# Kernel tuning notes

Hardware: AMD Instinct MI355X
Metric: run time of the kernel (lower is better)

The kernel has to match this reference:

```python
import jax, jax.numpy as jnp
import numpy as np

G = 512      # number of structures (groups)
CNT = 8192   # residues per structure
S = 8192     # sampled pairs per structure (self.samples)
N = G * CNT  # total residues


def _sample_pairs():
    # Deterministic replication of StochasticRGNLoss.pairs: per-group randint
    # sampling, with group offsets added so indices address the global array.
    rng = np.random.default_rng(0)
    local = rng.integers(0, CNT, size=(G, S, 2))
    # avoid degenerate left==right pairs (zero distance -> NaN grad of norm)
    eq = local[..., 0] == local[..., 1]
    local[..., 1] = np.where(eq, (local[..., 1] + 1) % CNT, local[..., 1])
    offs = (np.arange(G) * CNT)[:, None, None]
    pairs = (local + offs).reshape(-1, 2)
    return pairs[:, 0].astype(np.int32), pairs[:, 1].astype(np.int32)


def setup_inputs() -> dict:
    key = jax.random.key(0)
    k1, k2 = jax.random.split(key)
    inputs = jax.random.normal(k1, (N, 3, 3), dtype=jnp.float32)
    target = jax.random.normal(k2, (N, 3, 3), dtype=jnp.float32)
    left_np, right_np = _sample_pairs()
    return {
        "inputs": inputs,
        "target": target,
        "left": jnp.asarray(left_np),
        "right": jnp.asarray(right_np),
    }


def reference(inputs, target, left, right):
    # take the CA atom (index 1) of each residue frame -> [N, 3]
    ca_in = inputs[:, 1]
    ca_tg = target[:, 1]
    # irregular gather of sampled pairs, pairwise distances -> [P]
    d_in = jnp.linalg.norm(ca_in[left] - ca_in[right], axis=1)
    d_tg = jnp.linalg.norm(ca_tg[left] - ca_tg[right], axis=1)
    return jnp.mean((d_in - d_tg) ** 2)
```

## Files before the change

kernel.cpp:

```cpp
#include <hip/hip_runtime.h>

#define G_GROUPS 512
#define CNT      8192
#define S_PAIRS  8192
#define BLOCK    1024

union F4H {
    float4   f;
    _Float16 h[8];
};

__global__ __launch_bounds__(BLOCK) void rgn_loss_kernel(
    const float* __restrict__ inputs,
    const float* __restrict__ target,
    const int*   __restrict__ left,
    const int*   __restrict__ right,
    float*       __restrict__ out)
{
    __shared__ float4 pts[CNT];
    __shared__ float  red[BLOCK / 64];

    const int g   = blockIdx.x;
    const int tid = threadIdx.x;
    const int gbase = g * CNT;

    for (int p = tid; p < CNT; p += BLOCK) {
        const size_t rec = (size_t)(gbase + p) * 9 + 3;
        const float* pin = inputs + rec;
        const float* ptg = target + rec;
        F4H u;
        u.h[0] = (_Float16)pin[0];
        u.h[1] = (_Float16)pin[1];
        u.h[2] = (_Float16)pin[2];
        u.h[3] = (_Float16)ptg[0];
        u.h[4] = (_Float16)ptg[1];
        u.h[5] = (_Float16)ptg[2];
        u.h[6] = (_Float16)0.0f;
        u.h[7] = (_Float16)0.0f;
        pts[p] = u.f;
    }
    __syncthreads();

    const size_t pbase = (size_t)g * S_PAIRS;
    float acc = 0.0f;
    for (int k = tid; k < S_PAIRS; k += BLOCK) {
        const int li = left [pbase + k] - gbase;
        const int ri = right[pbase + k] - gbase;
        F4H L, R;
        L.f = pts[li];
        R.f = pts[ri];
        const float dix = (float)L.h[0] - (float)R.h[0];
        const float diy = (float)L.h[1] - (float)R.h[1];
        const float diz = (float)L.h[2] - (float)R.h[2];
        const float dtx = (float)L.h[3] - (float)R.h[3];
        const float dty = (float)L.h[4] - (float)R.h[4];
        const float dtz = (float)L.h[5] - (float)R.h[5];
        const float din = sqrtf(dix * dix + diy * diy + diz * diz);
        const float dtg = sqrtf(dtx * dtx + dty * dty + dtz * dtz);
        const float d   = din - dtg;
        acc += d * d;
    }

    const int lane = tid & 63;
    const int wid  = tid >> 6;
    #pragma unroll
    for (int off = 32; off > 0; off >>= 1)
        acc += __shfl_down(acc, off);
    if (lane == 0) red[wid] = acc;
    __syncthreads();
    if (wid == 0) {
        float v = (lane < BLOCK / 64) ? red[lane] : 0.0f;
        #pragma unroll
        for (int off = 8; off > 0; off >>= 1)
            v += __shfl_down(v, off);
        if (lane == 0)
            atomicAdd(out, v * (1.0f / ((float)G_GROUPS * (float)S_PAIRS)));
    }
}

extern "C" void kernel_launch(void* const* d_in, const int* in_sizes, int n_in,
                              void* d_out, int out_size, void* d_ws, size_t ws_size,
                              hipStream_t stream) {
    const float* inputs = (const float*)d_in[0];
    const float* target = (const float*)d_in[1];
    const int*   left   = (const int*)d_in[2];
    const int*   right  = (const int*)d_in[3];
    float*       out    = (float*)d_out;

    hipMemsetAsync(out, 0, sizeof(float), stream);
    rgn_loss_kernel<<<G_GROUPS, BLOCK, 0, stream>>>(inputs, target, left, right, out);
}
```

Before: 334.4 us.

## Stage residue records via coalesced float4 loads through per-wave LDS bounce buffer

Each wave now loads whole 9-float residue records as contiguous float4 chunks, stages them in a per-wave shared-memory bounce buffer, and extracts the CA coordinates from there. The old path issued strided scalar loads. The point table is packed to 6 halves (12 bytes) per residue instead of 16, which shrinks LDS. Pair indices are prefetched into registers before staging so their latency overlaps the gather. In exchange the kernel reads the full 36-byte records, including unused atoms, and the bounce buffer uses more LDS. The packed layout also needs three 4-byte LDS reads per point instead of one 16-byte read.

```diff
diff --git a/kernel.cpp b/kernel.cpp
--- a/kernel.cpp
+++ b/kernel.cpp
@@ -4,72 +4,99 @@
 #define CNT      8192
 #define S_PAIRS  8192
 #define BLOCK    1024
+#define WAVES    (BLOCK / 64)
+#define REC_PER_WAVE (CNT / WAVES)
+#define SUB_REC  64
+#define SUB_ITERS (REC_PER_WAVE / SUB_REC)
+#define SUB_F4   (SUB_REC * 9 / 4)
+#define PAIRS_PER_THREAD (S_PAIRS / BLOCK)
 
-union F4H {
-    float4   f;
-    _Float16 h[8];
+union U2H {
+    unsigned int u;
+    _Float16     h[2];
 };
 
 __global__ __launch_bounds__(BLOCK) void rgn_loss_kernel(
-    const float* __restrict__ inputs,
-    const float* __restrict__ target,
-    const int*   __restrict__ left,
-    const int*   __restrict__ right,
-    float*       __restrict__ out)
+    const float4* __restrict__ inputs4,
+    const float4* __restrict__ target4,
+    const int*    __restrict__ left,
+    const int*    __restrict__ right,
+    float*        __restrict__ out)
 {
-    __shared__ float4 pts[CNT];
-    __shared__ float  red[BLOCK / 64];
+    __shared__ _Float16 ptsH[CNT * 6];
+    __shared__ float4 bounce4[WAVES * SUB_F4];
+    __shared__ float red[WAVES];
 
-    const int g   = blockIdx.x;
-    const int tid = threadIdx.x;
+    const int tid  = threadIdx.x;
+    const int lane = tid & 63;
+    const int wid  = tid >> 6;
+    const int g    = blockIdx.x;
     const int gbase = g * CNT;
 
-    for (int p = tid; p < CNT; p += BLOCK) {
-        const size_t rec = (size_t)(gbase + p) * 9 + 3;
-        const float* pin = inputs + rec;
-        const float* ptg = target + rec;
-        F4H u;
-        u.h[0] = (_Float16)pin[0];
-        u.h[1] = (_Float16)pin[1];
-        u.h[2] = (_Float16)pin[2];
-        u.h[3] = (_Float16)ptg[0];
-        u.h[4] = (_Float16)ptg[1];
-        u.h[5] = (_Float16)ptg[2];
-        u.h[6] = (_Float16)0.0f;
-        u.h[7] = (_Float16)0.0f;
-        pts[p] = u.f;
+    const size_t pbase = (size_t)g * S_PAIRS;
+    int li[PAIRS_PER_THREAD], ri[PAIRS_PER_THREAD];
+    #pragma unroll
+    for (int i = 0; i < PAIRS_PER_THREAD; ++i) {
+        li[i] = left [pbase + tid + i * BLOCK] - gbase;
+        ri[i] = right[pbase + tid + i * BLOCK] - gbase;
+    }
+
+    float4* myb4 = &bounce4[wid * SUB_F4];
+    const float* myb = (const float*)myb4;
+
+    #pragma unroll
+    for (int t = 0; t < 2; ++t) {
+        const float4* src = (t == 0) ? inputs4 : target4;
+        const size_t wbase_f4 = ((size_t)gbase + (size_t)wid * REC_PER_WAVE) * 9 / 4;
+        for (int s = 0; s < SUB_ITERS; ++s) {
+            const size_t cbase = wbase_f4 + (size_t)s * SUB_F4;
+            float4 v0 = src[cbase + lane];
+            float4 v1 = src[cbase + lane + 64];
+            float4 v2;
+            if (lane < SUB_F4 - 128) v2 = src[cbase + lane + 128];
+            myb4[lane]      = v0;
+            myb4[lane + 64] = v1;
+            if (lane < SUB_F4 - 128) myb4[lane + 128] = v2;
+            const float x = myb[9 * lane + 3];
+            const float y = myb[9 * lane + 4];
+            const float z = myb[9 * lane + 5];
+            const int p = wid * REC_PER_WAVE + s * SUB_REC + lane;
+            _Float16* dst = &ptsH[p * 6 + t * 3];
+            dst[0] = (_Float16)x;
+            dst[1] = (_Float16)y;
+            dst[2] = (_Float16)z;
+        }
     }
     __syncthreads();
 
-    const size_t pbase = (size_t)g * S_PAIRS;
+    const unsigned int* ptsU = (const unsigned int*)ptsH;
     float acc = 0.0f;
-    for (int k = tid; k < S_PAIRS; k += BLOCK) {
-        const int li = left [pbase + k] - gbase;
-        const int ri = right[pbase + k] - gbase;
-        F4H L, R;
-        L.f = pts[li];
-        R.f = pts[ri];
-        const float dix = (float)L.h[0] - (float)R.h[0];
-        const float diy = (float)L.h[1] - (float)R.h[1];
-        const float diz = (float)L.h[2] - (float)R.h[2];
-        const float dtx = (float)L.h[3] - (float)R.h[3];
-        const float dty = (float)L.h[4] - (float)R.h[4];
-        const float dtz = (float)L.h[5] - (float)R.h[5];
+    #pragma unroll
+    for (int i = 0; i < PAIRS_PER_THREAD; ++i) {
+        const int l3 = li[i] * 3;
+        const int r3 = ri[i] * 3;
+        U2H L0, L1, L2, R0, R1, R2;
+        L0.u = ptsU[l3];     L1.u = ptsU[l3 + 1]; L2.u = ptsU[l3 + 2];
+        R0.u = ptsU[r3];     R1.u = ptsU[r3 + 1]; R2.u = ptsU[r3 + 2];
+        const float dix = (float)L0.h[0] - (float)R0.h[0];
+        const float diy = (float)L0.h[1] - (float)R0.h[1];
+        const float diz = (float)L1.h[0] - (float)R1.h[0];
+        const float dtx = (float)L1.h[1] - (float)R1.h[1];
+        const float dty = (float)L2.h[0] - (float)R2.h[0];
+        const float dtz = (float)L2.h[1] - (float)R2.h[1];
         const float din = sqrtf(dix * dix + diy * diy + diz * diz);
         const float dtg = sqrtf(dtx * dtx + dty * dty + dtz * dtz);
         const float d   = din - dtg;
         acc += d * d;
     }
 
-    const int lane = tid & 63;
-    const int wid  = tid >> 6;
     #pragma unroll
     for (int off = 32; off > 0; off >>= 1)
         acc += __shfl_down(acc, off);
     if (lane == 0) red[wid] = acc;
     __syncthreads();
     if (wid == 0) {
-        float v = (lane < BLOCK / 64) ? red[lane] : 0.0f;
+        float v = (lane < WAVES) ? red[lane] : 0.0f;
         #pragma unroll
         for (int off = 8; off > 0; off >>= 1)
             v += __shfl_down(v, off);
@@ -81,11 +108,11 @@
 extern "C" void kernel_launch(void* const* d_in, const int* in_sizes, int n_in,
                               void* d_out, int out_size, void* d_ws, size_t ws_size,
                               hipStream_t stream) {
-    const float* inputs = (const float*)d_in[0];
-    const float* target = (const float*)d_in[1];
-    const int*   left   = (const int*)d_in[2];
-    const int*   right  = (const int*)d_in[3];
-    float*       out    = (float*)d_out;
+    const float4* inputs = (const float4*)d_in[0];
+    const float4* target = (const float4*)d_in[1];
+    const int*    left   = (const int*)d_in[2];
+    const int*    right  = (const int*)d_in[3];
+    float*        out    = (float*)d_out;
 
     hipMemsetAsync(out, 0, sizeof(float), stream);
     rgn_loss_kernel<<<G_GROUPS, BLOCK, 0, stream>>>(inputs, target, left, right, out);
```

Result: no change. 338.9 us (+1.3%).

## Stage CA coordinates into LDS via direct global-to-LDS loads in two phases

Applied to the files above, without the earlier changes.

Replaces the per-thread scalar loads plus fp16 packing with __builtin_amdgcn_global_load_lds 16-byte copies of the CA record (reading 4 floats, one spilling past the CA triple) straight into shared memory, first for inputs, then reusing the same table for target. Pair indices are prefetched into registers before staging so their latency overlaps the table fill. This removes the fp16 conversion, keeping full fp32 precision, and halves the scalar load instructions, at the cost of extra barriers and serialising the two table phases. The 16-byte reads are unaligned (offset 12 bytes times 9-float stride), which the direct-to-LDS path may or may not support correctly.

```diff
diff --git a/kernel.cpp b/kernel.cpp
--- a/kernel.cpp
+++ b/kernel.cpp
@@ -4,11 +4,13 @@
 #define CNT      8192
 #define S_PAIRS  8192
 #define BLOCK    1024
+#define WAVES    (BLOCK / 64)
+#define RPW      (CNT / WAVES)
+#define CHUNKS   (RPW / 64)
+#define PPT      (S_PAIRS / BLOCK)
 
-union F4H {
-    float4   f;
-    _Float16 h[8];
-};
+typedef __attribute__((address_space(3))) void  lds_void;
+typedef const __attribute__((address_space(1))) void g_void;
 
 __global__ __launch_bounds__(BLOCK) void rgn_loss_kernel(
     const float* __restrict__ inputs,
@@ -17,59 +19,80 @@
     const int*   __restrict__ right,
     float*       __restrict__ out)
 {
-    __shared__ float4 pts[CNT];
-    __shared__ float  red[BLOCK / 64];
+    __shared__ float4 tab4[CNT];
+    __shared__ float  red[WAVES];
 
-    const int g   = blockIdx.x;
-    const int tid = threadIdx.x;
+    const int tid   = threadIdx.x;
+    const int lane  = tid & 63;
+    const int wid   = tid >> 6;
+    const int g     = blockIdx.x;
     const int gbase = g * CNT;
 
-    for (int p = tid; p < CNT; p += BLOCK) {
-        const size_t rec = (size_t)(gbase + p) * 9 + 3;
-        const float* pin = inputs + rec;
-        const float* ptg = target + rec;
-        F4H u;
-        u.h[0] = (_Float16)pin[0];
-        u.h[1] = (_Float16)pin[1];
-        u.h[2] = (_Float16)pin[2];
-        u.h[3] = (_Float16)ptg[0];
-        u.h[4] = (_Float16)ptg[1];
-        u.h[5] = (_Float16)ptg[2];
-        u.h[6] = (_Float16)0.0f;
-        u.h[7] = (_Float16)0.0f;
-        pts[p] = u.f;
+    const size_t pbase = (size_t)g * S_PAIRS;
+    int li[PPT], ri[PPT];
+    #pragma unroll
+    for (int i = 0; i < PPT; ++i) {
+        li[i] = left [pbase + tid + i * BLOCK] - gbase;
+        ri[i] = right[pbase + tid + i * BLOCK] - gbase;
+    }
+
+    {
+        const int rbase = wid * RPW;
+        #pragma unroll
+        for (int c = 0; c < CHUNKS; ++c) {
+            const int r = rbase + c * 64;
+            const float* gp = inputs + (size_t)(gbase + r + lane) * 9 + 3;
+            __builtin_amdgcn_global_load_lds((g_void*)gp,
+                                             (lds_void*)&tab4[r],
+                                             16, 0, 0);
+        }
     }
     __syncthreads();
 
-    const size_t pbase = (size_t)g * S_PAIRS;
+    float din[PPT];
+    #pragma unroll
+    for (int i = 0; i < PPT; ++i) {
+        const float4 L = tab4[li[i]];
+        const float4 R = tab4[ri[i]];
+        const float dx = L.x - R.x;
+        const float dy = L.y - R.y;
+        const float dz = L.z - R.z;
+        din[i] = sqrtf(dx * dx + dy * dy + dz * dz);
+    }
+    __syncthreads();
+
+    {
+        const int rbase = wid * RPW;
+        #pragma unroll
+        for (int c = 0; c < CHUNKS; ++c) {
+            const int r = rbase + c * 64;
+            const float* gp = target + (size_t)(gbase + r + lane) * 9 + 3;
+            __builtin_amdgcn_global_load_lds((g_void*)gp,
+                                             (lds_void*)&tab4[r],
+                                             16, 0, 0);
+        }
+    }
+    __syncthreads();
+
     float acc = 0.0f;
-    for (int k = tid; k < S_PAIRS; k += BLOCK) {
-        const int li = left [pbase + k] - gbase;
-        const int ri = right[pbase + k] - gbase;
-        F4H L, R;
-        L.f = pts[li];
-        R.f = pts[ri];
-        const float dix = (float)L.h[0] - (float)R.h[0];
-        const float diy = (float)L.h[1] - (float)R.h[1];
-        const float diz = (float)L.h[2] - (float)R.h[2];
-        const float dtx = (float)L.h[3] - (float)R.h[3];
-        const float dty = (float)L.h[4] - (float)R.h[4];
-        const float dtz = (float)L.h[5] - (float)R.h[5];
-        const float din = sqrtf(dix * dix + diy * diy + diz * diz);
-        const float dtg = sqrtf(dtx * dtx + dty * dty + dtz * dtz);
-        const float d   = din - dtg;
+    #pragma unroll
+    for (int i = 0; i < PPT; ++i) {
+        const float4 L = tab4[li[i]];
+        const float4 R = tab4[ri[i]];
+        const float dx = L.x - R.x;
+        const float dy = L.y - R.y;
+        const float dz = L.z - R.z;
+        const float d  = din[i] - sqrtf(dx * dx + dy * dy + dz * dz);
         acc += d * d;
     }
 
-    const int lane = tid & 63;
-    const int wid  = tid >> 6;
     #pragma unroll
     for (int off = 32; off > 0; off >>= 1)
         acc += __shfl_down(acc, off);
     if (lane == 0) red[wid] = acc;
     __syncthreads();
     if (wid == 0) {
-        float v = (lane < BLOCK / 64) ? red[lane] : 0.0f;
+        float v = (lane < WAVES) ? red[lane] : 0.0f;
         #pragma unroll
         for (int off = 8; off > 0; off >>= 1)
             v += __shfl_down(v, off);
```

Result: no change. 331.1 us (-1.0%).
